# Optimization experiments

Hardware: AMD Instinct MI355X
Metric: run time of the kernel (lower is better)

## Reference

```python
import jax, jax.numpy as jnp
import numpy as np

N_NODES = 100000
N_EDGES = 1600000
IN_DIM = 128
HID_DIM = 64
OUT_DIM = 1


def setup_inputs() -> dict:
    key = jax.random.key(0)
    k = jax.random.split(key, 8)
    x = jax.random.normal(k[0], (N_NODES, IN_DIM), dtype=jnp.float32)
    edge_index = jax.random.randint(k[1], (2, N_EDGES), 0, N_NODES, dtype=jnp.int64)
    # GCNConv layer 1: weight [IN, HID], bias [HID] (glorot-ish scale)
    W1 = jax.random.normal(k[2], (IN_DIM, HID_DIM), dtype=jnp.float32) / np.sqrt(IN_DIM)
    b1 = jnp.zeros((HID_DIM,), dtype=jnp.float32)
    W2 = jax.random.normal(k[3], (HID_DIM, HID_DIM), dtype=jnp.float32) / np.sqrt(HID_DIM)
    b2 = jnp.zeros((HID_DIM,), dtype=jnp.float32)
    Wfc = jax.random.normal(k[4], (HID_DIM, OUT_DIM), dtype=jnp.float32) / np.sqrt(HID_DIM)
    bfc = jnp.zeros((OUT_DIM,), dtype=jnp.float32)
    return {"x": x, "edge_index": edge_index, "W1": W1, "b1": b1,
            "W2": W2, "b2": b2, "Wfc": Wfc, "bfc": bfc}


def _gcn_norm(edge_index, n_nodes):
    # PyG GCNConv default: add self-loops, symmetric normalization.
    src, dst = edge_index[0], edge_index[1]
    loop = jnp.arange(n_nodes, dtype=src.dtype)
    src = jnp.concatenate([src, loop])
    dst = jnp.concatenate([dst, loop])
    deg = jax.ops.segment_sum(jnp.ones_like(dst, dtype=jnp.float32), dst,
                              num_segments=n_nodes)
    deg_isqrt = jax.lax.rsqrt(deg)  # deg >= 1 thanks to self-loops
    norm = deg_isqrt[src] * deg_isqrt[dst]  # [E+N]
    return src, dst, norm


def _gcn_conv(x, src, dst, norm, W, b, n_nodes):
    h = x @ W                      # [N, D_out] dense transform first (D_out <= D_in)
    msg = h[src] * norm[:, None]   # gather + normalize  [E+N, D_out]
    out = jax.ops.segment_sum(msg, dst, num_segments=n_nodes)  # scatter-add
    return out + b


def reference(x, edge_index, W1, b1, W2, b2, Wfc, bfc):
    n = x.shape[0]
    src, dst, norm = _gcn_norm(edge_index, n)
    h = jax.nn.relu(_gcn_conv(x, src, dst, norm, W1, b1, n))
    h = jax.nn.relu(_gcn_conv(h, src, dst, norm, W2, b2, n))
    return h @ Wfc + bfc  # [N, 1]
```

## Files before the change

### kernel.cpp

```cpp
#include <hip/hip_runtime.h>
#include <hip/hip_bf16.h>


#define IN_DIM 128
#define HID 64
#define B1 256
#define MAXNC 128

typedef unsigned int uint;

__device__ inline uint pack_bf16x2(float a, float b) {
    uint ua = __builtin_bit_cast(uint, a);
    uint ub = __builtin_bit_cast(uint, b);
    ua += 0x7fffu + ((ua >> 16) & 1u);
    ub += 0x7fffu + ((ub >> 16) & 1u);
    return (ua >> 16) | (ub & 0xffff0000u);
}
__device__ inline float bf_lo(uint g) { return __builtin_bit_cast(float, g << 16); }
__device__ inline float bf_hi(uint g) { return __builtin_bit_cast(float, g & 0xffff0000u); }

__global__ __launch_bounds__(512) void hist1(const int* __restrict__ dst,
                                             int* __restrict__ ghist,
                                             int E, int NC, int chunk) {
    __shared__ int h[MAXNC];
    int t = threadIdx.x, blk = blockIdx.x;
    if (t < NC) h[t] = 0;
    __syncthreads();
    int s = blk * chunk, e = min(E, s + chunk);
    for (int i = s + t; i < e; i += 512) atomicAdd(&h[dst[i] >> 10], 1);
    __syncthreads();
    if (t < NC) ghist[(size_t)t * B1 + blk] = h[t];
}

__global__ __launch_bounds__(1024) void scan_mat(int* __restrict__ a, int M,
                                                 int* __restrict__ row_off, int N) {
    __shared__ int ws[16], wsoff[16], total_s;
    int t = threadIdx.x;
    int seg = (M + 1023) >> 10;
    int s = t * seg, e = min(M, s + seg);
    int sum = 0;
    for (int i = s; i < e; ++i) sum += a[i];
    int incl = sum;
#pragma unroll
    for (int o = 1; o < 64; o <<= 1) {
        int u = __shfl_up(incl, o, 64);
        if ((t & 63) >= o) incl += u;
    }
    if ((t & 63) == 63) ws[t >> 6] = incl;
    __syncthreads();
    if (t == 0) {
        int run = 0;
#pragma unroll
        for (int i = 0; i < 16; ++i) { wsoff[i] = run; run += ws[i]; }
        total_s = run;
    }
    __syncthreads();
    int run = wsoff[t >> 6] + incl - sum;
    for (int i = s; i < e; ++i) { int tmp = a[i]; a[i] = run; run += tmp; }
    if (t == 0) row_off[N] = total_s;
}

__global__ __launch_bounds__(512) void scatter1(const int* __restrict__ src,
                                                const int* __restrict__ dst,
                                                const int* __restrict__ goff,
                                                uint* __restrict__ pairs,
                                                int E, int NC, int chunk) {
    __shared__ int cur[MAXNC];
    int t = threadIdx.x, blk = blockIdx.x;
    if (t < NC) cur[t] = goff[(size_t)t * B1 + blk];
    __syncthreads();
    int s = blk * chunk, e = min(E, s + chunk);
    for (int i = s + t; i < e; i += 512) {
        int d = dst[i];
        int p = atomicAdd(&cur[d >> 10], 1);
        pairs[p] = ((uint)src[i] << 10) | (uint)(d & 1023);
    }
}

__global__ __launch_bounds__(1024) void build_csr(const uint* __restrict__ pairs,
                                                  const int* __restrict__ goff,
                                                  int* __restrict__ row_off,
                                                  float* __restrict__ disqrt,
                                                  int* __restrict__ col,
                                                  int E, int NC, int N) {
    __shared__ int h[1024], cur[1024];
    __shared__ int ws[16], wsoff[16];
    int b = blockIdx.x, t = threadIdx.x;
    int base = goff[(size_t)b * B1];
    int next = (b + 1 < NC) ? goff[(size_t)(b + 1) * B1] : E;
    h[t] = 0;
    __syncthreads();
    for (int i = base + t; i < next; i += 1024)
        atomicAdd(&h[pairs[i] & 1023u], 1);
    __syncthreads();
    int deg = h[t];
    int incl = deg;
#pragma unroll
    for (int o = 1; o < 64; o <<= 1) {
        int u = __shfl_up(incl, o, 64);
        if ((t & 63) >= o) incl += u;
    }
    if ((t & 63) == 63) ws[t >> 6] = incl;
    __syncthreads();
    if (t == 0) {
        int run = 0;
#pragma unroll
        for (int i = 0; i < 16; ++i) { wsoff[i] = run; run += ws[i]; }
    }
    __syncthreads();
    int excl = wsoff[t >> 6] + incl - deg;
    cur[t] = base + excl;
    int node = (b << 10) + t;
    if (node < N) {
        row_off[node] = base + excl;
        disqrt[node]  = rsqrtf((float)(deg + 1));
    }
    __syncthreads();
    for (int i = base + t; i < next; i += 1024) {
        uint p = pairs[i];
        int pos = atomicAdd(&cur[p & 1023u], 1);
        col[pos] = (int)(p >> 10);
    }
}

template <int K>
__global__ __launch_bounds__(256) void gemm_tile(const float* __restrict__ X,
                                                 const float* __restrict__ W,
                                                 const float* __restrict__ disqrt,
                                                 uint* __restrict__ Tsb, int n) {
    __shared__ float xs[32][68];
    __shared__ float ws[32][64];
    const int tid  = threadIdx.x;
    const int nIdx = tid & 15;
    const int mIdx = tid >> 4;
    const int m0   = blockIdx.x * 64;
    const int r0 = tid >> 3, kq = tid & 7, r1 = r0 + 32;
    const int wk = tid >> 4, wc = tid & 15;
    const int row0 = m0 + r0, row1 = m0 + r1;
    const float4 z4 = make_float4(0.f, 0.f, 0.f, 0.f);

    float4 gx0 = (row0 < n) ? *(const float4*)(X + (size_t)row0 * K + 4 * kq) : z4;
    float4 gx1 = (row1 < n) ? *(const float4*)(X + (size_t)row1 * K + 4 * kq) : z4;
    float4 gw0 = *(const float4*)(W + (size_t)wk * 64 + 4 * wc);
    float4 gw1 = *(const float4*)(W + (size_t)(wk + 16) * 64 + 4 * wc);

    float acc[4][4] = {};
    for (int kc = 0;;) {
        xs[4 * kq + 0][r0] = gx0.x; xs[4 * kq + 1][r0] = gx0.y;
        xs[4 * kq + 2][r0] = gx0.z; xs[4 * kq + 3][r0] = gx0.w;
        xs[4 * kq + 0][r1] = gx1.x; xs[4 * kq + 1][r1] = gx1.y;
        xs[4 * kq + 2][r1] = gx1.z; xs[4 * kq + 3][r1] = gx1.w;
        *(float4*)&ws[wk][4 * wc]      = gw0;
        *(float4*)&ws[wk + 16][4 * wc] = gw1;
        __syncthreads();
        kc += 32;
        const bool more = kc < K;
        if (more) {
            gx0 = (row0 < n) ? *(const float4*)(X + (size_t)row0 * K + kc + 4 * kq) : z4;
            gx1 = (row1 < n) ? *(const float4*)(X + (size_t)row1 * K + kc + 4 * kq) : z4;
            gw0 = *(const float4*)(W + (size_t)(kc + wk) * 64 + 4 * wc);
            gw1 = *(const float4*)(W + (size_t)(kc + wk + 16) * 64 + 4 * wc);
        }
#pragma unroll 8
        for (int k = 0; k < 32; ++k) {
            float4 a = *(const float4*)&xs[k][4 * mIdx];
            float4 b = *(const float4*)&ws[k][4 * nIdx];
            const float* ap = (const float*)&a;
            const float* bp = (const float*)&b;
#pragma unroll
            for (int mi = 0; mi < 4; ++mi)
#pragma unroll
                for (int ni = 0; ni < 4; ++ni)
                    acc[mi][ni] += ap[mi] * bp[ni];
        }
        if (!more) break;
        __syncthreads();
    }
#pragma unroll
    for (int mi = 0; mi < 4; ++mi) {
        int row = m0 + 4 * mIdx + mi;
        if (row < n) {
            float s = disqrt[row];
            uint2 pk;
            pk.x = pack_bf16x2(acc[mi][0] * s, acc[mi][1] * s);
            pk.y = pack_bf16x2(acc[mi][2] * s, acc[mi][3] * s);
            *(uint2*)(Tsb + (size_t)row * 32 + 2 * nIdx) = pk;
        }
    }
}

template <bool FUSE_FC>
__global__ __launch_bounds__(256) void agg_kernel(const uint* __restrict__ Tsb,
                                                  const int* __restrict__ row_off,
                                                  const int* __restrict__ col,
                                                  const float* __restrict__ disqrt,
                                                  const float* __restrict__ bias,
                                                  const float* __restrict__ wfc,
                                                  const float* __restrict__ bfc,
                                                  float* __restrict__ out, int n) {
    int node = blockIdx.x * 4 + (threadIdx.x >> 6);
    if (node >= n) return;
    int lane = threadIdx.x & 63;
    int q = lane >> 4;
    int p = lane & 15;
    float4 acc = make_float4(0.f, 0.f, 0.f, 0.f);
    if (q == 0) {
        uint2 g = *(const uint2*)(Tsb + (size_t)node * 32 + 2 * p);
        acc.x = bf_lo(g.x); acc.y = bf_hi(g.x);
        acc.z = bf_lo(g.y); acc.w = bf_hi(g.y);
    }
    int beg = __builtin_amdgcn_readfirstlane(row_off[node]);
    int end = __builtin_amdgcn_readfirstlane(row_off[node + 1]);
    for (int batch = beg; batch < end; batch += 64) {
        int bn = min(64, end - batch);
        int cv = 0;
        if (batch + lane < end) cv = col[batch + lane];
        int j = 0;
        for (; j + 16 <= bn; j += 16) {
            int s0 = __shfl(cv, j + q, 64);
            int s1 = __shfl(cv, j + 4 + q, 64);
            int s2 = __shfl(cv, j + 8 + q, 64);
            int s3 = __shfl(cv, j + 12 + q, 64);
            uint2 g0 = *(const uint2*)(Tsb + (size_t)s0 * 32 + 2 * p);
            uint2 g1 = *(const uint2*)(Tsb + (size_t)s1 * 32 + 2 * p);
            uint2 g2 = *(const uint2*)(Tsb + (size_t)s2 * 32 + 2 * p);
            uint2 g3 = *(const uint2*)(Tsb + (size_t)s3 * 32 + 2 * p);
            acc.x += bf_lo(g0.x); acc.y += bf_hi(g0.x);
            acc.z += bf_lo(g0.y); acc.w += bf_hi(g0.y);
            acc.x += bf_lo(g1.x); acc.y += bf_hi(g1.x);
            acc.z += bf_lo(g1.y); acc.w += bf_hi(g1.y);
            acc.x += bf_lo(g2.x); acc.y += bf_hi(g2.x);
            acc.z += bf_lo(g2.y); acc.w += bf_hi(g2.y);
            acc.x += bf_lo(g3.x); acc.y += bf_hi(g3.x);
            acc.z += bf_lo(g3.y); acc.w += bf_hi(g3.y);
        }
        for (; j < bn; j += 4) {
            int idx = j + q;
            int s = __shfl(cv, idx & 63, 64);
            uint2 g = *(const uint2*)(Tsb + (size_t)s * 32 + 2 * p);
            if (idx < bn) {
                acc.x += bf_lo(g.x); acc.y += bf_hi(g.x);
                acc.z += bf_lo(g.y); acc.w += bf_hi(g.y);
            }
        }
    }
    acc.x += __shfl_xor(acc.x, 16, 64);
    acc.y += __shfl_xor(acc.y, 16, 64);
    acc.z += __shfl_xor(acc.z, 16, 64);
    acc.w += __shfl_xor(acc.w, 16, 64);
    acc.x += __shfl_xor(acc.x, 32, 64);
    acc.y += __shfl_xor(acc.y, 32, 64);
    acc.z += __shfl_xor(acc.z, 32, 64);
    acc.w += __shfl_xor(acc.w, 32, 64);
    float dq = disqrt[node];
    float4 bv = *(const float4*)(bias + 4 * p);
    float r0 = fmaxf(acc.x * dq + bv.x, 0.f);
    float r1 = fmaxf(acc.y * dq + bv.y, 0.f);
    float r2 = fmaxf(acc.z * dq + bv.z, 0.f);
    float r3 = fmaxf(acc.w * dq + bv.w, 0.f);
    if (!FUSE_FC) {
        if (q == 0)
            *(float4*)(out + (size_t)node * HID + 4 * p) =
                make_float4(r0, r1, r2, r3);
    } else {
        float4 wv = *(const float4*)(wfc + 4 * p);
        float v = r0 * wv.x + r1 * wv.y + r2 * wv.z + r3 * wv.w;
        v += __shfl_down(v, 8, 64);
        v += __shfl_down(v, 4, 64);
        v += __shfl_down(v, 2, 64);
        v += __shfl_down(v, 1, 64);
        if (lane == 0) out[node] = v + bfc[0];
    }
}

extern "C" void kernel_launch(void* const* d_in, const int* in_sizes, int n_in,
                              void* d_out, int out_size, void* d_ws, size_t ws_size,
                              hipStream_t stream) {
    const float* x   = (const float*)d_in[0];
    const int*   ei  = (const int*)d_in[1];
    const float* W1  = (const float*)d_in[2];
    const float* b1  = (const float*)d_in[3];
    const float* W2  = (const float*)d_in[4];
    const float* b2  = (const float*)d_in[5];
    const float* Wfc = (const float*)d_in[6];
    const float* bfc = (const float*)d_in[7];
    float* out = (float*)d_out;

    const int N = in_sizes[0] / IN_DIM;
    const int E = in_sizes[1] / 2;
    const int* src = ei;
    const int* dst = ei + E;
    const int NC    = (N + 1023) >> 10;
    const int chunk = (E + B1 - 1) / B1;

    char* w = (char*)d_ws;
    auto alloc = [&](size_t bytes) {
        void* p = (void*)w;
        w += (bytes + 255) & ~(size_t)255;
        return p;
    };
    int*   row_off = (int*)alloc((size_t)(N + 1) * 4);
    float* disqrt  = (float*)alloc((size_t)N * 4);
    int*   goff    = (int*)alloc((size_t)NC * B1 * 4);
    int*   col     = (int*)alloc((size_t)E * 4);
    size_t scrA = (size_t)E * 4, scrB = (size_t)N * HID * 2;
    void*  scr  = alloc(scrA > scrB ? scrA : scrB);
    float* h1   = (float*)alloc((size_t)N * HID * 4);
    uint*  pairs = (uint*)scr;
    uint*  Tsb   = (uint*)scr;

    hist1<<<B1, 512, 0, stream>>>(dst, goff, E, NC, chunk);
    scan_mat<<<1, 1024, 0, stream>>>(goff, NC * B1, row_off, N);
    scatter1<<<B1, 512, 0, stream>>>(src, dst, goff, pairs, E, NC, chunk);
    build_csr<<<NC, 1024, 0, stream>>>(pairs, goff, row_off, disqrt, col, E, NC, N);

    gemm_tile<IN_DIM><<<(N + 63) / 64, 256, 0, stream>>>(x, W1, disqrt, Tsb, N);
    agg_kernel<false><<<(N + 3) / 4, 256, 0, stream>>>(Tsb, row_off, col, disqrt,
                                                       b1, nullptr, nullptr, h1, N);

    gemm_tile<HID><<<(N + 63) / 64, 256, 0, stream>>>(h1, W2, disqrt, Tsb, N);
    agg_kernel<true><<<(N + 3) / 4, 256, 0, stream>>>(Tsb, row_off, col, disqrt,
                                                      b2, Wfc, bfc, out, N);
}
```

Baseline: 302.0 us.

## Store hidden layer in bf16 and widen aggregation gathers to 16-byte loads

The first aggregation now writes the hidden activations as packed bf16 instead of fp32, and a new GEMM variant reads that bf16 input directly, halving the traffic for the intermediate h1. The aggregation kernel is also restructured so each lane gathers 8 features with uint4 loads, and 8 neighbors are processed per step instead of 4, with a three-stage shuffle reduction. This adds extra rounding of h1 to bf16, a small accuracy risk, and raises per-lane register use.

After: 300.1 us. No clear change (-0.6%).

```diff
diff --git a/kernel.cpp b/kernel.cpp
--- a/kernel.cpp
+++ b/kernel.cpp
@@ -189,6 +189,72 @@
     }
 }
 
+__global__ __launch_bounds__(256) void gemm_tile_b(const uint* __restrict__ Xb,
+                                                   const float* __restrict__ W,
+                                                   const float* __restrict__ disqrt,
+                                                   uint* __restrict__ Tsb, int n) {
+    const int K = 64;
+    __shared__ float xs[32][68];
+    __shared__ float ws[32][64];
+    const int tid  = threadIdx.x;
+    const int nIdx = tid & 15;
+    const int mIdx = tid >> 4;
+    const int m0   = blockIdx.x * 64;
+    const int r0 = tid >> 3, kq = tid & 7, r1 = r0 + 32;
+    const int wk = tid >> 4, wc = tid & 15;
+    const int row0 = m0 + r0, row1 = m0 + r1;
+    const uint2 z2 = make_uint2(0u, 0u);
+
+    uint2 gx0 = (row0 < n) ? *(const uint2*)(Xb + (size_t)row0 * 32 + 2 * kq) : z2;
+    uint2 gx1 = (row1 < n) ? *(const uint2*)(Xb + (size_t)row1 * 32 + 2 * kq) : z2;
+    float4 gw0 = *(const float4*)(W + (size_t)wk * 64 + 4 * wc);
+    float4 gw1 = *(const float4*)(W + (size_t)(wk + 16) * 64 + 4 * wc);
+
+    float acc[4][4] = {};
+    for (int kc = 0;;) {
+        xs[4 * kq + 0][r0] = bf_lo(gx0.x); xs[4 * kq + 1][r0] = bf_hi(gx0.x);
+        xs[4 * kq + 2][r0] = bf_lo(gx0.y); xs[4 * kq + 3][r0] = bf_hi(gx0.y);
+        xs[4 * kq + 0][r1] = bf_lo(gx1.x); xs[4 * kq + 1][r1] = bf_hi(gx1.x);
+        xs[4 * kq + 2][r1] = bf_lo(gx1.y); xs[4 * kq + 3][r1] = bf_hi(gx1.y);
+        *(float4*)&ws[wk][4 * wc]      = gw0;
+        *(float4*)&ws[wk + 16][4 * wc] = gw1;
+        __syncthreads();
+        kc += 32;
+        const bool more = kc < K;
+        if (more) {
+            gx0 = (row0 < n) ? *(const uint2*)(Xb + (size_t)row0 * 32 + 16 + 2 * kq) : z2;
+            gx1 = (row1 < n) ? *(const uint2*)(Xb + (size_t)row1 * 32 + 16 + 2 * kq) : z2;
+            gw0 = *(const float4*)(W + (size_t)(kc + wk) * 64 + 4 * wc);
+            gw1 = *(const float4*)(W + (size_t)(kc + wk + 16) * 64 + 4 * wc);
+        }
+#pragma unroll 8
+        for (int k = 0; k < 32; ++k) {
+            float4 a = *(const float4*)&xs[k][4 * mIdx];
+            float4 b = *(const float4*)&ws[k][4 * nIdx];
+            const float* ap = (const float*)&a;
+            const float* bp = (const float*)&b;
+#pragma unroll
+            for (int mi = 0; mi < 4; ++mi)
+#pragma unroll
+                for (int ni = 0; ni < 4; ++ni)
+                    acc[mi][ni] += ap[mi] * bp[ni];
+        }
+        if (!more) break;
+        __syncthreads();
+    }
+#pragma unroll
+    for (int mi = 0; mi < 4; ++mi) {
+        int row = m0 + 4 * mIdx + mi;
+        if (row < n) {
+            float s = disqrt[row];
+            uint2 pk;
+            pk.x = pack_bf16x2(acc[mi][0] * s, acc[mi][1] * s);
+            pk.y = pack_bf16x2(acc[mi][2] * s, acc[mi][3] * s);
+            *(uint2*)(Tsb + (size_t)row * 32 + 2 * nIdx) = pk;
+        }
+    }
+}
+
 template <bool FUSE_FC>
 __global__ __launch_bounds__(256) void agg_kernel(const uint* __restrict__ Tsb,
                                                   const int* __restrict__ row_off,
@@ -197,17 +263,20 @@
                                                   const float* __restrict__ bias,
                                                   const float* __restrict__ wfc,
                                                   const float* __restrict__ bfc,
-                                                  float* __restrict__ out, int n) {
+                                                  uint* __restrict__ outb,
+                                                  float* __restrict__ outf, int n) {
     int node = blockIdx.x * 4 + (threadIdx.x >> 6);
     if (node >= n) return;
     int lane = threadIdx.x & 63;
-    int q = lane >> 4;
-    int p = lane & 15;
-    float4 acc = make_float4(0.f, 0.f, 0.f, 0.f);
-    if (q == 0) {
-        uint2 g = *(const uint2*)(Tsb + (size_t)node * 32 + 2 * p);
-        acc.x = bf_lo(g.x); acc.y = bf_hi(g.x);
-        acc.z = bf_lo(g.y); acc.w = bf_hi(g.y);
+    int o = lane >> 3;
+    int p = lane & 7;
+    float acc[8] = {};
+    if (o == 0) {
+        uint4 g = *(const uint4*)(Tsb + (size_t)node * 32 + 4 * p);
+        acc[0] = bf_lo(g.x); acc[1] = bf_hi(g.x);
+        acc[2] = bf_lo(g.y); acc[3] = bf_hi(g.y);
+        acc[4] = bf_lo(g.z); acc[5] = bf_hi(g.z);
+        acc[6] = bf_lo(g.w); acc[7] = bf_hi(g.w);
     }
     int beg = __builtin_amdgcn_readfirstlane(row_off[node]);
     int end = __builtin_amdgcn_readfirstlane(row_off[node + 1]);
@@ -217,59 +286,67 @@
         if (batch + lane < end) cv = col[batch + lane];
         int j = 0;
         for (; j + 16 <= bn; j += 16) {
-            int s0 = __shfl(cv, j + q, 64);
-            int s1 = __shfl(cv, j + 4 + q, 64);
-            int s2 = __shfl(cv, j + 8 + q, 64);
-            int s3 = __shfl(cv, j + 12 + q, 64);
-            uint2 g0 = *(const uint2*)(Tsb + (size_t)s0 * 32 + 2 * p);
-            uint2 g1 = *(const uint2*)(Tsb + (size_t)s1 * 32 + 2 * p);
-            uint2 g2 = *(const uint2*)(Tsb + (size_t)s2 * 32 + 2 * p);
-            uint2 g3 = *(const uint2*)(Tsb + (size_t)s3 * 32 + 2 * p);
-            acc.x += bf_lo(g0.x); acc.y += bf_hi(g0.x);
-            acc.z += bf_lo(g0.y); acc.w += bf_hi(g0.y);
-            acc.x += bf_lo(g1.x); acc.y += bf_hi(g1.x);
-            acc.z += bf_lo(g1.y); acc.w += bf_hi(g1.y);
-            acc.x += bf_lo(g2.x); acc.y += bf_hi(g2.x);
-            acc.z += bf_lo(g2.y); acc.w += bf_hi(g2.y);
-            acc.x += bf_lo(g3.x); acc.y += bf_hi(g3.x);
-            acc.z += bf_lo(g3.y); acc.w += bf_hi(g3.y);
-        }
-        for (; j < bn; j += 4) {
-            int idx = j + q;
+            int s0 = __shfl(cv, j + o, 64);
+            int s1 = __shfl(cv, j + 8 + o, 64);
+            uint4 g0 = *(const uint4*)(Tsb + (size_t)s0 * 32 + 4 * p);
+            uint4 g1 = *(const uint4*)(Tsb + (size_t)s1 * 32 + 4 * p);
+            acc[0] += bf_lo(g0.x); acc[1] += bf_hi(g0.x);
+            acc[2] += bf_lo(g0.y); acc[3] += bf_hi(g0.y);
+            acc[4] += bf_lo(g0.z); acc[5] += bf_hi(g0.z);
+            acc[6] += bf_lo(g0.w); acc[7] += bf_hi(g0.w);
+            acc[0] += bf_lo(g1.x); acc[1] += bf_hi(g1.x);
+            acc[2] += bf_lo(g1.y); acc[3] += bf_hi(g1.y);
+            acc[4] += bf_lo(g1.z); acc[5] += bf_hi(g1.z);
+            acc[6] += bf_lo(g1.w); acc[7] += bf_hi(g1.w);
+        }
+        for (; j < bn; j += 8) {
+            int idx = j + o;
             int s = __shfl(cv, idx & 63, 64);
-            uint2 g = *(const uint2*)(Tsb + (size_t)s * 32 + 2 * p);
+            uint4 g = *(const uint4*)(Tsb + (size_t)s * 32 + 4 * p);
             if (idx < bn) {
-                acc.x += bf_lo(g.x); acc.y += bf_hi(g.x);
-                acc.z += bf_lo(g.y); acc.w += bf_hi(g.y);
+                acc[0] += bf_lo(g.x); acc[1] += bf_hi(g.x);
+                acc[2] += bf_lo(g.y); acc[3] += bf_hi(g.y);
+                acc[4] += bf_lo(g.z); acc[5] += bf_hi(g.z);
+                acc[6] += bf_lo(g.w); acc[7] += bf_hi(g.w);
             }
         }
     }
-    acc.x += __shfl_xor(acc.x, 16, 64);
-    acc.y += __shfl_xor(acc.y, 16, 64);
-    acc.z += __shfl_xor(acc.z, 16, 64);
-    acc.w += __shfl_xor(acc.w, 16, 64);
-    acc.x += __shfl_xor(acc.x, 32, 64);
-    acc.y += __shfl_xor(acc.y, 32, 64);
-    acc.z += __shfl_xor(acc.z, 32, 64);
-    acc.w += __shfl_xor(acc.w, 32, 64);
+#pragma unroll
+    for (int k = 0; k < 8; ++k) {
+        acc[k] += __shfl_xor(acc[k], 8, 64);
+        acc[k] += __shfl_xor(acc[k], 16, 64);
+        acc[k] += __shfl_xor(acc[k], 32, 64);
+    }
     float dq = disqrt[node];
-    float4 bv = *(const float4*)(bias + 4 * p);
-    float r0 = fmaxf(acc.x * dq + bv.x, 0.f);
-    float r1 = fmaxf(acc.y * dq + bv.y, 0.f);
-    float r2 = fmaxf(acc.z * dq + bv.z, 0.f);
-    float r3 = fmaxf(acc.w * dq + bv.w, 0.f);
+    float4 bv0 = *(const float4*)(bias + 8 * p);
+    float4 bv1 = *(const float4*)(bias + 8 * p + 4);
+    float r[8];
+    r[0] = fmaxf(acc[0] * dq + bv0.x, 0.f);
+    r[1] = fmaxf(acc[1] * dq + bv0.y, 0.f);
+    r[2] = fmaxf(acc[2] * dq + bv0.z, 0.f);
+    r[3] = fmaxf(acc[3] * dq + bv0.w, 0.f);
+    r[4] = fmaxf(acc[4] * dq + bv1.x, 0.f);
+    r[5] = fmaxf(acc[5] * dq + bv1.y, 0.f);
+    r[6] = fmaxf(acc[6] * dq + bv1.z, 0.f);
+    r[7] = fmaxf(acc[7] * dq + bv1.w, 0.f);
     if (!FUSE_FC) {
-        if (q == 0)
-            *(float4*)(out + (size_t)node * HID + 4 * p) =
-                make_float4(r0, r1, r2, r3);
+        if (o == 0) {
+            uint4 pk;
+            pk.x = pack_bf16x2(r[0], r[1]);
+            pk.y = pack_bf16x2(r[2], r[3]);
+            pk.z = pack_bf16x2(r[4], r[5]);
+            pk.w = pack_bf16x2(r[6], r[7]);
+            *(uint4*)(outb + (size_t)node * 32 + 4 * p) = pk;
+        }
     } else {
-        float4 wv = *(const float4*)(wfc + 4 * p);
-        float v = r0 * wv.x + r1 * wv.y + r2 * wv.z + r3 * wv.w;
-        v += __shfl_down(v, 8, 64);
+        float4 wv0 = *(const float4*)(wfc + 8 * p);
+        float4 wv1 = *(const float4*)(wfc + 8 * p + 4);
+        float v = r[0] * wv0.x + r[1] * wv0.y + r[2] * wv0.z + r[3] * wv0.w +
+                  r[4] * wv1.x + r[5] * wv1.y + r[6] * wv1.z + r[7] * wv1.w;
         v += __shfl_down(v, 4, 64);
         v += __shfl_down(v, 2, 64);
         v += __shfl_down(v, 1, 64);
-        if (lane == 0) out[node] = v + bfc[0];
+        if (lane == 0) outf[node] = v + bfc[0];
     }
 }
 
@@ -305,7 +382,7 @@
     int*   col     = (int*)alloc((size_t)E * 4);
     size_t scrA = (size_t)E * 4, scrB = (size_t)N * HID * 2;
     void*  scr  = alloc(scrA > scrB ? scrA : scrB);
-    float* h1   = (float*)alloc((size_t)N * HID * 4);
+    uint*  h1b  = (uint*)alloc((size_t)N * HID * 2);
     uint*  pairs = (uint*)scr;
     uint*  Tsb   = (uint*)scr;
 
@@ -316,9 +393,11 @@
 
     gemm_tile<IN_DIM><<<(N + 63) / 64, 256, 0, stream>>>(x, W1, disqrt, Tsb, N);
     agg_kernel<false><<<(N + 3) / 4, 256, 0, stream>>>(Tsb, row_off, col, disqrt,
-                                                       b1, nullptr, nullptr, h1, N);
-
-    gemm_tile<HID><<<(N + 63) / 64, 256, 0, stream>>>(h1, W2, disqrt, Tsb, N);
+                                                       b1, nullptr, nullptr,
+                                                       h1b, nullptr, N);
+
+    gemm_tile_b<<<(N + 63) / 64, 256, 0, stream>>>(h1b, W2, disqrt, Tsb, N);
     agg_kernel<true><<<(N + 3) / 4, 256, 0, stream>>>(Tsb, row_off, col, disqrt,
-                                                      b2, Wfc, bfc, out, N);
-}
+                                                      b2, Wfc, bfc,
+                                                      nullptr, out, N);
+}
```
